# Kernel tuning notes

Measured on AMD Instinct MI355X. Metric: run time of the kernel, lower is better.

## Reference

```python
import jax, jax.numpy as jnp
import numpy as np

RADIUS_IN = 0.05
RADIUS_OUT = 0.2
NSAMPLE = 32


def setup_inputs() -> dict:
    key = jax.random.key(0)
    k1, k2, k3 = jax.random.split(key, 3)
    B, N, M, C = 2, 16384, 2048, 64
    xyz = jax.random.uniform(k1, (B, N, 3), dtype=jnp.float32)
    new_xyz = jax.random.uniform(k2, (B, M, 3), dtype=jnp.float32)
    features = jax.random.normal(k3, (B, C, N), dtype=jnp.float32)
    return {"xyz": xyz, "new_xyz": new_xyz, "features": features}


def _ball_query_dilated(xyz, new_xyz, r_in, r_out, nsample):
    # xyz: (B,N,3), new_xyz: (B,M,3)
    d2 = jnp.sum((new_xyz[:, :, None, :] - xyz[:, None, :, :]) ** 2, axis=-1)  # (B,M,N)
    mask = (d2 >= r_in * r_in) & (d2 < r_out * r_out)  # dilated shell
    B, M, N = mask.shape
    rank = jnp.cumsum(mask, axis=-1) - 1  # order of each match along N
    cnt = jnp.minimum(jnp.sum(mask, axis=-1), nsample).astype(jnp.int32)  # (B,M)
    # scatter the j-th point index into slot `rank` (overflow slots dumped into pad)
    pos = jnp.where(mask & (rank < nsample), rank, nsample)
    b = jnp.arange(B)[:, None, None]
    m = jnp.arange(M)[None, :, None]
    j = jnp.broadcast_to(jnp.arange(N, dtype=jnp.int32)[None, None, :], (B, M, N))
    idx = jnp.zeros((B, M, nsample + 1), jnp.int32).at[b, m, pos].set(j)[..., :nsample]
    # CUDA kernel fills unused slots with the FIRST matched index (0 if no match)
    slot = jnp.arange(nsample)[None, None, :]
    idx = jnp.where(slot < cnt[..., None], idx, idx[..., :1])
    return cnt, idx


def _group(features, idx):
    # features: (B,C,N), idx: (B,M,S) -> (B,C,M,S)
    B, C, N = features.shape
    _, M, S = idx.shape
    flat = idx.reshape(B, 1, M * S)
    return jnp.take_along_axis(features, flat, axis=2).reshape(B, C, M, S)


def reference(xyz, new_xyz, features):
    idx_cnt, idx = _ball_query_dilated(xyz, new_xyz, RADIUS_IN, RADIUS_OUT, NSAMPLE)
    xyz_t = jnp.transpose(xyz, (0, 2, 1))            # (B,3,N)
    grouped_xyz = _group(xyz_t, idx)                 # (B,3,M,S)
    grouped_xyz = grouped_xyz - jnp.transpose(new_xyz, (0, 2, 1))[..., None]
    grouped_features = _group(features, idx)         # (B,C,M,S)
    new_features = jnp.concatenate([grouped_xyz, grouped_features], axis=1)
    return idx_cnt, new_features
```

## Files before the change

### kernel.cpp

```cpp
#include <hip/hip_runtime.h>
#include <cstdint>

#define BB 2
#define NN 16384
#define MM 2048
#define CC 64
#define SS 32
#define WPB 4

__device__ __forceinline__ float dist2(float qx, float qy, float qz,
                                       float px, float py, float pz) {
    float dx = __fsub_rn(qx, px), dy = __fsub_rn(qy, py), dz = __fsub_rn(qz, pz);
    return __fadd_rn(__fadd_rn(__fmul_rn(dx, dx), __fmul_rn(dy, dy)), __fmul_rn(dz, dz));
}

__global__ __launch_bounds__(256) void prep_fused(
    const float* __restrict__ xyz, const float* __restrict__ f,
    float* __restrict__ ft, float4* __restrict__ xyz4) {
    int bid = blockIdx.x;
    if (bid < 2048) {
        __shared__ float tile[32][33];
        int n0 = (bid & 511) * 32;
        int c0 = ((bid >> 9) & 1) * 32;
        int b = bid >> 10;
        int tx = threadIdx.x & 31, ty = threadIdx.x >> 5;
#pragma unroll
        for (int k = 0; k < 32; k += 8)
            tile[ty + k][tx] = f[((size_t)(b * CC + c0 + ty + k)) * NN + n0 + tx];
        __syncthreads();
#pragma unroll
        for (int k = 0; k < 32; k += 8)
            ft[((size_t)(b * NN + n0 + ty + k)) * CC + c0 + tx] = tile[tx][ty + k];
    } else {
        int i = (bid - 2048) * 256 + threadIdx.x;
        if (i < BB * NN) {
            xyz4[i] = make_float4(xyz[3 * i], xyz[3 * i + 1], xyz[3 * i + 2], 0.f);
        }
    }
}

template <bool FAST>
__global__ __launch_bounds__(64 * WPB) void query_group(
    const float* __restrict__ xyz, const float* __restrict__ new_xyz,
    const float* __restrict__ features, const float* __restrict__ feat_t,
    const float4* __restrict__ xyz4, float* __restrict__ out) {
    constexpr float R_IN2 = 0.05f * 0.05f;
    constexpr float R_OUT2 = 0.2f * 0.2f;
    __shared__ int idxS[WPB][SS];
    __shared__ float fbuf[WPB][SS][CC + 4];

    int lane = threadIdx.x & 63;
    int w = threadIdx.x >> 6;
    int bm = blockIdx.x * WPB + w;
    int b = bm >> 11;
    int m = bm & 2047;

    float qx = new_xyz[(size_t)bm * 3 + 0];
    float qy = new_xyz[(size_t)bm * 3 + 1];
    float qz = new_xyz[(size_t)bm * 3 + 2];

    if (lane == 0) idxS[w][0] = 0;

    unsigned long long below = (1ull << lane) - 1ull;
    int cnt = 0;
    for (int j0 = 0; j0 < NN; j0 += 256) {
        float px[4], py[4], pz[4];
        if (FAST) {
            const float4* base = xyz4 + b * NN + j0 + lane;
#pragma unroll
            for (int u = 0; u < 4; ++u) {
                float4 p = base[u * 64];
                px[u] = p.x; py[u] = p.y; pz[u] = p.z;
            }
        } else {
            const float* pp = xyz + ((size_t)(b * NN + j0 + lane)) * 3;
#pragma unroll
            for (int u = 0; u < 4; ++u) {
                px[u] = pp[u * 192 + 0];
                py[u] = pp[u * 192 + 1];
                pz[u] = pp[u * 192 + 2];
            }
        }
#pragma unroll
        for (int u = 0; u < 4; ++u) {
            float d2 = dist2(qx, qy, qz, px[u], py[u], pz[u]);
            bool inshell = (d2 >= R_IN2) && (d2 < R_OUT2);
            unsigned long long mk = __ballot(inshell);
            if (inshell) {
                int r = cnt + __popcll(mk & below);
                if (r < SS) idxS[w][r] = j0 + u * 64 + lane;
            }
            cnt += __popcll(mk);
        }
        if (cnt >= SS) break;
    }
    if (cnt > SS) cnt = SS;
    if (lane == 0) out[bm] = (float)cnt;

    float* gout = out + BB * MM;

    if (FAST) {
        int s4 = lane >> 4, c4 = lane & 15;
        int jj[8];
#pragma unroll
        for (int it = 0; it < 8; ++it) {
            int sl = it * 4 + s4;
            jj[it] = (sl < cnt) ? idxS[w][sl] : idxS[w][0];
        }
        float4 vv[8];
#pragma unroll
        for (int it = 0; it < 8; ++it)
            vv[it] = ((const float4*)(feat_t + ((size_t)b * NN + jj[it]) * CC))[c4];
#pragma unroll
        for (int it = 0; it < 8; ++it)
            *((float4*)&fbuf[w][it * 4 + s4][c4 * 4]) = vv[it];
    }

    {
        int s = lane & 31, half = lane >> 5;
        int j = (s < cnt) ? idxS[w][s] : idxS[w][0];
        float px, py, pz;
        if (FAST) {
            float4 p = xyz4[b * NN + j];
            px = p.x; py = p.y; pz = p.z;
        } else {
            const float* pp = xyz + ((size_t)(b * NN) + j) * 3;
            px = pp[0]; py = pp[1]; pz = pp[2];
        }
        float v01 = half ? __fsub_rn(py, qy) : __fsub_rn(px, qx);
        gout[((size_t)(b * 67 + half) * MM + m) * SS + s] = v01;
        if (half == 0) {
            gout[((size_t)(b * 67 + 2) * MM + m) * SS + s] = __fsub_rn(pz, qz);
        }
    }

    if (FAST) {
        int ch8 = lane >> 3, sg = lane & 7;
#pragma unroll
        for (int it = 0; it < 8; ++it) {
            int ch = it * 8 + ch8;
            float4 v = make_float4(fbuf[w][sg * 4 + 0][ch], fbuf[w][sg * 4 + 1][ch],
                                   fbuf[w][sg * 4 + 2][ch], fbuf[w][sg * 4 + 3][ch]);
            *((float4*)&gout[((size_t)(b * 67 + 3 + ch) * MM + m) * SS + sg * 4]) = v;
        }
    } else {
        int s = lane & 31, half = lane >> 5;
        int j = (s < cnt) ? idxS[w][s] : idxS[w][0];
#pragma unroll
        for (int k = 0; k < 32; ++k) {
            int ch = 2 * k + half;
            float v = features[((size_t)(b * CC + ch)) * NN + j];
            gout[((size_t)(b * 67 + 3 + ch) * MM + m) * SS + s] = v;
        }
    }
}

extern "C" void kernel_launch(void* const* d_in, const int* in_sizes, int n_in,
                              void* d_out, int out_size, void* d_ws, size_t ws_size,
                              hipStream_t stream) {
    const float* xyz = (const float*)d_in[0];
    const float* new_xyz = (const float*)d_in[1];
    const float* features = (const float*)d_in[2];
    float* out = (float*)d_out;

    const size_t featT_bytes = (size_t)BB * NN * CC * 4;
    const size_t xyz4_bytes = (size_t)BB * NN * 16;
    bool fast = ws_size >= featT_bytes + xyz4_bytes;

    if (fast) {
        float* feat_t = (float*)d_ws;
        float4* xyz4 = (float4*)((char*)d_ws + featT_bytes);
        prep_fused<<<2048 + 128, 256, 0, stream>>>(xyz, features, feat_t, xyz4);
        query_group<true><<<BB * MM / WPB, 64 * WPB, 0, stream>>>(xyz, new_xyz, features, feat_t, xyz4, out);
    } else {
        query_group<false><<<BB * MM / WPB, 64 * WPB, 0, stream>>>(xyz, new_xyz, features, nullptr, nullptr, out);
    }
}
```

Baseline: 92.20 us.

## Split into scan, bounded transpose and group kernels to skip unused features

The fused query/group kernel is split into three kernels. A scan kernel writes neighbour indices to workspace and uses an atomic max to record the furthest point index any query needed. A transpose kernel then converts only the feature columns below that bound, and a group kernel gathers from the transposed features. The aim is to avoid transposing feature columns that early-exiting queries never reach, and the padded xyz4 copy is dropped. The costs are an extra launch, a round trip of the index array through global memory, and a scan that now reads strided AoS xyz. The max cell is never reset between calls, so it can only stay at or above the bound the current inputs need.

```diff
diff --git a/kernel.cpp b/kernel.cpp
--- a/kernel.cpp
+++ b/kernel.cpp
@@ -8,52 +8,25 @@
 #define SS 32
 #define WPB 4
 
+
 __device__ __forceinline__ float dist2(float qx, float qy, float qz,
                                        float px, float py, float pz) {
     float dx = __fsub_rn(qx, px), dy = __fsub_rn(qy, py), dz = __fsub_rn(qz, pz);
     return __fadd_rn(__fadd_rn(__fmul_rn(dx, dx), __fmul_rn(dy, dy)), __fmul_rn(dz, dz));
 }
 
-__global__ __launch_bounds__(256) void prep_fused(
-    const float* __restrict__ xyz, const float* __restrict__ f,
-    float* __restrict__ ft, float4* __restrict__ xyz4) {
-    int bid = blockIdx.x;
-    if (bid < 2048) {
-        __shared__ float tile[32][33];
-        int n0 = (bid & 511) * 32;
-        int c0 = ((bid >> 9) & 1) * 32;
-        int b = bid >> 10;
-        int tx = threadIdx.x & 31, ty = threadIdx.x >> 5;
-#pragma unroll
-        for (int k = 0; k < 32; k += 8)
-            tile[ty + k][tx] = f[((size_t)(b * CC + c0 + ty + k)) * NN + n0 + tx];
-        __syncthreads();
-#pragma unroll
-        for (int k = 0; k < 32; k += 8)
-            ft[((size_t)(b * NN + n0 + ty + k)) * CC + c0 + tx] = tile[tx][ty + k];
-    } else {
-        int i = (bid - 2048) * 256 + threadIdx.x;
-        if (i < BB * NN) {
-            xyz4[i] = make_float4(xyz[3 * i], xyz[3 * i + 1], xyz[3 * i + 2], 0.f);
-        }
-    }
-}
-
-template <bool FAST>
-__global__ __launch_bounds__(64 * WPB) void query_group(
+__global__ __launch_bounds__(64 * WPB) void scan_kernel(
     const float* __restrict__ xyz, const float* __restrict__ new_xyz,
-    const float* __restrict__ features, const float* __restrict__ feat_t,
-    const float4* __restrict__ xyz4, float* __restrict__ out) {
+    int* __restrict__ idx_all, int* __restrict__ maxj_cell,
+    float* __restrict__ out) {
     constexpr float R_IN2 = 0.05f * 0.05f;
     constexpr float R_OUT2 = 0.2f * 0.2f;
     __shared__ int idxS[WPB][SS];
-    __shared__ float fbuf[WPB][SS][CC + 4];
 
     int lane = threadIdx.x & 63;
     int w = threadIdx.x >> 6;
     int bm = blockIdx.x * WPB + w;
     int b = bm >> 11;
-    int m = bm & 2047;
 
     float qx = new_xyz[(size_t)bm * 3 + 0];
     float qy = new_xyz[(size_t)bm * 3 + 1];
@@ -63,23 +36,15 @@
 
     unsigned long long below = (1ull << lane) - 1ull;
     int cnt = 0;
+    int j_exit = NN;
     for (int j0 = 0; j0 < NN; j0 += 256) {
         float px[4], py[4], pz[4];
-        if (FAST) {
-            const float4* base = xyz4 + b * NN + j0 + lane;
-#pragma unroll
-            for (int u = 0; u < 4; ++u) {
-                float4 p = base[u * 64];
-                px[u] = p.x; py[u] = p.y; pz[u] = p.z;
-            }
-        } else {
-            const float* pp = xyz + ((size_t)(b * NN + j0 + lane)) * 3;
-#pragma unroll
-            for (int u = 0; u < 4; ++u) {
-                px[u] = pp[u * 192 + 0];
-                py[u] = pp[u * 192 + 1];
-                pz[u] = pp[u * 192 + 2];
-            }
+        const float* pp = xyz + ((size_t)(b * NN + j0 + lane)) * 3;
+#pragma unroll
+        for (int u = 0; u < 4; ++u) {
+            px[u] = pp[u * 192 + 0];
+            py[u] = pp[u * 192 + 1];
+            pz[u] = pp[u * 192 + 2];
         }
 #pragma unroll
         for (int u = 0; u < 4; ++u) {
@@ -92,41 +57,76 @@
             }
             cnt += __popcll(mk);
         }
-        if (cnt >= SS) break;
+        if (cnt >= SS) { j_exit = j0 + 256; break; }
     }
     if (cnt > SS) cnt = SS;
-    if (lane == 0) out[bm] = (float)cnt;
+    if (lane == 0) {
+        out[bm] = (float)cnt;
+        atomicMax(maxj_cell, j_exit);
+    }
+    if (lane < SS) {
+        int j = (lane < cnt) ? idxS[w][lane] : idxS[w][0];
+        idx_all[bm * SS + lane] = j;
+    }
+}
+
+__global__ __launch_bounds__(256) void transpose_bounded(
+    const float* __restrict__ f, float* __restrict__ ft,
+    const int* __restrict__ maxj_cell) {
+    int limit = *maxj_cell;
+    int bid = blockIdx.x;
+    int n0 = (bid & 511) * 32;
+    if (n0 >= limit) return;
+    int c0 = ((bid >> 9) & 1) * 32;
+    int b = bid >> 10;
+    __shared__ float tile[32][33];
+    int tx = threadIdx.x & 31, ty = threadIdx.x >> 5;
+#pragma unroll
+    for (int k = 0; k < 32; k += 8)
+        tile[ty + k][tx] = f[((size_t)(b * CC + c0 + ty + k)) * NN + n0 + tx];
+    __syncthreads();
+#pragma unroll
+    for (int k = 0; k < 32; k += 8)
+        ft[((size_t)(b * NN + n0 + ty + k)) * CC + c0 + tx] = tile[tx][ty + k];
+}
+
+__global__ __launch_bounds__(64 * WPB) void group_kernel(
+    const float* __restrict__ xyz, const float* __restrict__ new_xyz,
+    const float* __restrict__ feat_t, const int* __restrict__ idx_all,
+    float* __restrict__ out) {
+    __shared__ int idxS[WPB][SS];
+    __shared__ float fbuf[WPB][SS][CC + 4];
+
+    int lane = threadIdx.x & 63;
+    int w = threadIdx.x >> 6;
+    int bm = blockIdx.x * WPB + w;
+    int b = bm >> 11;
+    int m = bm & 2047;
+
+    if (lane < SS) idxS[w][lane] = idx_all[bm * SS + lane];
 
     float* gout = out + BB * MM;
 
-    if (FAST) {
-        int s4 = lane >> 4, c4 = lane & 15;
-        int jj[8];
-#pragma unroll
-        for (int it = 0; it < 8; ++it) {
-            int sl = it * 4 + s4;
-            jj[it] = (sl < cnt) ? idxS[w][sl] : idxS[w][0];
-        }
-        float4 vv[8];
-#pragma unroll
-        for (int it = 0; it < 8; ++it)
-            vv[it] = ((const float4*)(feat_t + ((size_t)b * NN + jj[it]) * CC))[c4];
-#pragma unroll
-        for (int it = 0; it < 8; ++it)
-            *((float4*)&fbuf[w][it * 4 + s4][c4 * 4]) = vv[it];
-    }
+    int s4 = lane >> 4, c4 = lane & 15;
+    int jj[8];
+#pragma unroll
+    for (int it = 0; it < 8; ++it) jj[it] = idxS[w][it * 4 + s4];
+    float4 vv[8];
+#pragma unroll
+    for (int it = 0; it < 8; ++it)
+        vv[it] = ((const float4*)(feat_t + ((size_t)b * NN + jj[it]) * CC))[c4];
+#pragma unroll
+    for (int it = 0; it < 8; ++it)
+        *((float4*)&fbuf[w][it * 4 + s4][c4 * 4]) = vv[it];
 
     {
         int s = lane & 31, half = lane >> 5;
-        int j = (s < cnt) ? idxS[w][s] : idxS[w][0];
-        float px, py, pz;
-        if (FAST) {
-            float4 p = xyz4[b * NN + j];
-            px = p.x; py = p.y; pz = p.z;
-        } else {
-            const float* pp = xyz + ((size_t)(b * NN) + j) * 3;
-            px = pp[0]; py = pp[1]; pz = pp[2];
-        }
+        int j = idxS[w][s];
+        const float* pp = xyz + ((size_t)(b * NN) + j) * 3;
+        float px = pp[0], py = pp[1], pz = pp[2];
+        float qx = new_xyz[(size_t)bm * 3 + 0];
+        float qy = new_xyz[(size_t)bm * 3 + 1];
+        float qz = new_xyz[(size_t)bm * 3 + 2];
         float v01 = half ? __fsub_rn(py, qy) : __fsub_rn(px, qx);
         gout[((size_t)(b * 67 + half) * MM + m) * SS + s] = v01;
         if (half == 0) {
@@ -134,7 +134,7 @@
         }
     }
 
-    if (FAST) {
+    {
         int ch8 = lane >> 3, sg = lane & 7;
 #pragma unroll
         for (int it = 0; it < 8; ++it) {
@@ -143,15 +143,68 @@
                                    fbuf[w][sg * 4 + 2][ch], fbuf[w][sg * 4 + 3][ch]);
             *((float4*)&gout[((size_t)(b * 67 + 3 + ch) * MM + m) * SS + sg * 4]) = v;
         }
-    } else {
-        int s = lane & 31, half = lane >> 5;
-        int j = (s < cnt) ? idxS[w][s] : idxS[w][0];
-#pragma unroll
-        for (int k = 0; k < 32; ++k) {
-            int ch = 2 * k + half;
-            float v = features[((size_t)(b * CC + ch)) * NN + j];
-            gout[((size_t)(b * 67 + 3 + ch) * MM + m) * SS + s] = v;
-        }
+    }
+}
+
+__global__ __launch_bounds__(64 * WPB) void query_group_fallback(
+    const float* __restrict__ xyz, const float* __restrict__ new_xyz,
+    const float* __restrict__ features, float* __restrict__ out) {
+    constexpr float R_IN2 = 0.05f * 0.05f;
+    constexpr float R_OUT2 = 0.2f * 0.2f;
+    __shared__ int idxS[WPB][SS];
+
+    int lane = threadIdx.x & 63;
+    int w = threadIdx.x >> 6;
+    int bm = blockIdx.x * WPB + w;
+    int b = bm >> 11;
+    int m = bm & 2047;
+
+    float qx = new_xyz[(size_t)bm * 3 + 0];
+    float qy = new_xyz[(size_t)bm * 3 + 1];
+    float qz = new_xyz[(size_t)bm * 3 + 2];
+
+    if (lane == 0) idxS[w][0] = 0;
+
+    unsigned long long below = (1ull << lane) - 1ull;
+    int cnt = 0;
+    for (int j0 = 0; j0 < NN; j0 += 256) {
+        float px[4], py[4], pz[4];
+        const float* pp = xyz + ((size_t)(b * NN + j0 + lane)) * 3;
+#pragma unroll
+        for (int u = 0; u < 4; ++u) {
+            px[u] = pp[u * 192 + 0];
+            py[u] = pp[u * 192 + 1];
+            pz[u] = pp[u * 192 + 2];
+        }
+#pragma unroll
+        for (int u = 0; u < 4; ++u) {
+            float d2 = dist2(qx, qy, qz, px[u], py[u], pz[u]);
+            bool inshell = (d2 >= R_IN2) && (d2 < R_OUT2);
+            unsigned long long mk = __ballot(inshell);
+            if (inshell) {
+                int r = cnt + __popcll(mk & below);
+                if (r < SS) idxS[w][r] = j0 + u * 64 + lane;
+            }
+            cnt += __popcll(mk);
+        }
+        if (cnt >= SS) break;
+    }
+    if (cnt > SS) cnt = SS;
+    if (lane == 0) out[bm] = (float)cnt;
+
+    float* gout = out + BB * MM;
+    int s = lane & 31, half = lane >> 5;
+    int j = (s < cnt) ? idxS[w][s] : idxS[w][0];
+    const float* pp = xyz + ((size_t)(b * NN) + j) * 3;
+    float px = pp[0], py = pp[1], pz = pp[2];
+    float v01 = half ? __fsub_rn(py, qy) : __fsub_rn(px, qx);
+    gout[((size_t)(b * 67 + half) * MM + m) * SS + s] = v01;
+    if (half == 0) gout[((size_t)(b * 67 + 2) * MM + m) * SS + s] = __fsub_rn(pz, qz);
+#pragma unroll
+    for (int k = 0; k < 32; ++k) {
+        int ch = 2 * k + half;
+        float v = features[((size_t)(b * CC + ch)) * NN + j];
+        gout[((size_t)(b * 67 + 3 + ch) * MM + m) * SS + s] = v;
     }
 }
 
@@ -164,15 +217,17 @@
     float* out = (float*)d_out;
 
     const size_t featT_bytes = (size_t)BB * NN * CC * 4;
-    const size_t xyz4_bytes = (size_t)BB * NN * 16;
-    bool fast = ws_size >= featT_bytes + xyz4_bytes;
+    const size_t idx_bytes = (size_t)BB * MM * SS * 4;
+    bool fast = ws_size >= featT_bytes + idx_bytes + 4;
 
     if (fast) {
         float* feat_t = (float*)d_ws;
-        float4* xyz4 = (float4*)((char*)d_ws + featT_bytes);
-        prep_fused<<<2048 + 128, 256, 0, stream>>>(xyz, features, feat_t, xyz4);
-        query_group<true><<<BB * MM / WPB, 64 * WPB, 0, stream>>>(xyz, new_xyz, features, feat_t, xyz4, out);
+        int* idx_all = (int*)((char*)d_ws + featT_bytes);
+        int* maxj_cell = (int*)((char*)d_ws + featT_bytes + idx_bytes);
+        scan_kernel<<<BB * MM / WPB, 64 * WPB, 0, stream>>>(xyz, new_xyz, idx_all, maxj_cell, out);
+        transpose_bounded<<<2048, 256, 0, stream>>>(features, feat_t, maxj_cell);
+        group_kernel<<<BB * MM / WPB, 64 * WPB, 0, stream>>>(xyz, new_xyz, feat_t, idx_all, out);
     } else {
-        query_group<false><<<BB * MM / WPB, 64 * WPB, 0, stream>>>(xyz, new_xyz, features, nullptr, nullptr, out);
-    }
-}
+        query_group_fallback<<<BB * MM / WPB, 64 * WPB, 0, stream>>>(xyz, new_xyz, features, out);
+    }
+}
```

Result: slower. 136.7 us (+48.3%).
